# Optimization experiments

Measured on AMD Instinct MI355X. Metric: run time of the kernel, lower is better.

Reference implementation:

```python
import jax, jax.numpy as jnp
import numpy as np

N_NODES = 100000
N_EDGES = 1600000
IN_DIM, HID_DIM, OUT_DIM = 128, 32, 32


def setup_inputs() -> dict:
    key = jax.random.key(0)
    k1, k2, k3, k4, k5 = jax.random.split(key, 5)
    x = jax.random.normal(k1, (N_NODES, IN_DIM), dtype=jnp.float32)
    W1 = jax.random.normal(k2, (IN_DIM, HID_DIM), dtype=jnp.float32) * (1.0 / np.sqrt(IN_DIM))
    W2 = jax.random.normal(k3, (HID_DIM, OUT_DIM), dtype=jnp.float32) * (1.0 / np.sqrt(HID_DIM))
    edge_weight = jax.random.uniform(k4, (N_EDGES,), dtype=jnp.float32)
    edge_index = jax.random.randint(k5, (2, N_EDGES), 0, N_NODES, dtype=jnp.int64)
    return {"x": x, "W1": W1, "W2": W2, "edge_weight": edge_weight, "edge_index": edge_index}


def _gcn_conv(x, W, edge_index, edge_weight):
    # GCNConv with add_self_loops=False, normalize=False, bias=False:
    # h = x @ W ; out[dst] += edge_weight * h[src]
    src, dst = edge_index[0], edge_index[1]
    h = x @ W                                   # [N, out]
    msg = h[src] * edge_weight[:, None]         # [E, out] gather + scale
    return jax.ops.segment_sum(msg, dst, num_segments=x.shape[0])  # scatter-add


def reference(x, W1, W2, edge_weight, edge_index):
    h = _gcn_conv(x, W1, edge_index, edge_weight)   # no activation in source
    z = _gcn_conv(h, W2, edge_index, edge_weight)
    return z
```

## Files before the change

kernel.cpp:

```cpp
#include <hip/hip_runtime.h>

#define N_NODES 100000
#define N_EDGES 1600000
#define IN_DIM 128
#define HID_DIM 32

#define NPB 256
#define BSHIFT 8
#define NBUCK ((N_NODES + NPB - 1) / NPB)
#define EPB 4096
#define NBLK_E ((N_EDGES + EPB - 1) / EPB)
#define OSTRIDE (NBUCK + 1)
#define CAPB 4608
#define MMROWS 128
#define NBLK_MM ((N_NODES + MMROWS - 1) / MMROWS)
#define MM1 352
#define MM2 (NBLK_MM - MM1)
#define XS_STRIDE 136

typedef __attribute__((ext_vector_type(8))) short bf16x8;
typedef __attribute__((ext_vector_type(4))) float f32x4;

__device__ __forceinline__ unsigned int pack_bf16x2(float a0, float a1) {
    unsigned int u0 = __float_as_uint(a0), u1 = __float_as_uint(a1);
    u0 = (u0 + 0x7FFFu + ((u0 >> 16) & 1u)) >> 16;
    u1 = (u1 + 0x7FFFu + ((u1 >> 16) & 1u)) >> 16;
    return u0 | (u1 << 16);
}

__device__ __forceinline__ unsigned short bf16_of(float v) {
    unsigned int u = __float_as_uint(v);
    u = (u + 0x7FFFu + ((u >> 16) & 1u)) >> 16;
    return (unsigned short)u;
}

__device__ __forceinline__ int scan512(int v, int* wtmp) {
    const int t = threadIdx.x, lane = t & 63, wv = t >> 6;
    int incl = v;
#pragma unroll
    for (int o = 1; o < 64; o <<= 1) {
        const int n = __shfl_up(incl, o, 64);
        if (lane >= o) incl += n;
    }
    if (lane == 63) wtmp[wv] = incl;
    __syncthreads();
    if (t < 8) {
        const int wval = wtmp[t];
        int s = wval;
#pragma unroll
        for (int o = 1; o < 8; o <<= 1) {
            const int n = __shfl_up(s, o, 64);
            if (t >= o) s += n;
        }
        wtmp[t] = s - wval;
    }
    __syncthreads();
    return incl + wtmp[wv];
}

__device__ __forceinline__ void mm_body(char* smem, int row0,
                                        const float* __restrict__ x,
                                        const float* __restrict__ W,
                                        unsigned int* __restrict__ h) {
    const int tid = threadIdx.x;
    unsigned short* xbf = (unsigned short*)smem;
    const int lane = tid & 63, w = tid >> 6;

#pragma unroll
    for (int i = 0; i < 8; ++i) {
        const int idx = tid + i * 512;
        const int r = idx >> 5, c4 = idx & 31;
        const int grow = row0 + r;
        float4 vv = (grow < N_NODES) ? ((const float4*)x)[(size_t)grow * 32 + c4]
                                     : make_float4(0.f, 0.f, 0.f, 0.f);
        *(uint2*)&xbf[r * XS_STRIDE + c4 * 4] =
            make_uint2(pack_bf16x2(vv.x, vv.y), pack_bf16x2(vv.z, vv.w));
    }

    const int colB = lane & 15, kg = lane >> 4;
    bf16x8 bfrag[2][4];
#pragma unroll
    for (int n = 0; n < 2; ++n)
#pragma unroll
        for (int kt = 0; kt < 4; ++kt) {
            const int kbase = kt * 32 + kg * 8;
            bf16x8 f;
#pragma unroll
            for (int j = 0; j < 8; ++j)
                f[j] = (short)bf16_of(W[(size_t)(kbase + j) * HID_DIM + n * 16 + colB]);
            bfrag[n][kt] = f;
        }
    __syncthreads();

    f32x4 acc0 = {0.f, 0.f, 0.f, 0.f}, acc1 = {0.f, 0.f, 0.f, 0.f};
    const int arow = w * 16 + (lane & 15);
#pragma unroll
    for (int kt = 0; kt < 4; ++kt) {
        bf16x8 a = *(bf16x8*)&xbf[arow * XS_STRIDE + kt * 32 + kg * 8];
        acc0 = __builtin_amdgcn_mfma_f32_16x16x32_bf16(a, bfrag[0][kt], acc0, 0, 0, 0);
        acc1 = __builtin_amdgcn_mfma_f32_16x16x32_bf16(a, bfrag[1][kt], acc1, 0, 0, 0);
    }
    __syncthreads();

    float* cst = (float*)smem;
    float* cw_ = cst + w * 576;
    const int crow = (lane >> 4) * 4;
#pragma unroll
    for (int r = 0; r < 4; ++r) {
        cw_[(crow + r) * 36 + (lane & 15)] = acc0[r];
        cw_[(crow + r) * 36 + 16 + (lane & 15)] = acc1[r];
    }
    __syncthreads();
    const int r = tid >> 2, q = tid & 3;
    const int grow = row0 + r;
    if (grow < N_NODES) {
        const float* cr = cst + (r >> 4) * 576 + (r & 15) * 36 + q * 8;
        uint4 o = make_uint4(pack_bf16x2(cr[0], cr[1]), pack_bf16x2(cr[2], cr[3]),
                             pack_bf16x2(cr[4], cr[5]), pack_bf16x2(cr[6], cr[7]));
        ((uint4*)h)[(size_t)grow * 4 + q] = o;
    }
}

__global__ __launch_bounds__(512) void fusedA(const int* __restrict__ ei,
                                              const float* __restrict__ ew,
                                              unsigned int* __restrict__ ulin,
                                              unsigned short* __restrict__ wlin,
                                              int* __restrict__ ostart,
                                              const float* __restrict__ x,
                                              const float* __restrict__ W,
                                              unsigned int* __restrict__ h) {
    __shared__ __align__(16) char smem[36000];
    const int tid = threadIdx.x;

    if (blockIdx.x < NBLK_E) {
        unsigned int*   stag_u = (unsigned int*)smem;
        unsigned short* stag_w = (unsigned short*)(smem + 16384);
        int* lh     = (int*)(smem + 24576);
        int* lstart = (int*)(smem + 26144);
        int* wtmp   = (int*)(smem + 27712);

        for (int j = tid; j < NBUCK; j += 512) lh[j] = 0;
        __syncthreads();

        const int e0 = blockIdx.x * EPB;
        int dstr[8];
        unsigned int srcr[8];
        unsigned short wreg[8];
#pragma unroll
        for (int u = 0; u < 8; ++u) {
            const int e = e0 + u * 512 + tid;
            if (e < N_EDGES) {
                dstr[u] = ei[N_EDGES + e];
                srcr[u] = (unsigned int)ei[e];
                wreg[u] = bf16_of(ew[e]);
                atomicAdd(&lh[dstr[u] >> BSHIFT], 1);
            } else {
                dstr[u] = -1; srcr[u] = 0; wreg[u] = 0;
            }
        }
        __syncthreads();

        const int v = (tid < NBUCK) ? lh[tid] : 0;
        const int incl = scan512(v, wtmp);
        if (tid < NBUCK) lstart[tid] = incl - v;
        if (tid == NBUCK - 1) lstart[NBUCK] = incl;
        __syncthreads();
        if (tid < NBUCK) lh[tid] = 0;
        __syncthreads();

#pragma unroll
        for (int u = 0; u < 8; ++u) {
            const int d = dstr[u];
            if (d >= 0) {
                const int b = d >> BSHIFT;
                const int slot = atomicAdd(&lh[b], 1);
                const int p = lstart[b] + slot;
                stag_u[p] = srcr[u] | ((unsigned int)(d & (NPB - 1)) << 17);
                stag_w[p] = wreg[u];
            }
        }
        __syncthreads();

        const int total = lstart[NBUCK];
        const size_t gbase = (size_t)blockIdx.x * EPB;
        for (int i = tid; i < total; i += 512) {
            ulin[gbase + i] = stag_u[i];
            wlin[gbase + i] = stag_w[i];
        }
        if (tid < OSTRIDE) ostart[blockIdx.x * OSTRIDE + tid] = lstart[tid];
    } else {
        mm_body(smem, (int)(blockIdx.x - NBLK_E) * MMROWS, x, W, h);
    }
}

__global__ __launch_bounds__(512) void fusedB(const int* __restrict__ ostart,
                                              const unsigned int* __restrict__ ulin,
                                              const unsigned short* __restrict__ wlin,
                                              unsigned int* __restrict__ csr,
                                              int* __restrict__ offs,
                                              const float* __restrict__ x,
                                              const float* __restrict__ W,
                                              unsigned int* __restrict__ h) {
    __shared__ __align__(16) char smem[50304];
    const int t = threadIdx.x;

    if (blockIdx.x < NBUCK) {
        unsigned int*   stag_u = (unsigned int*)smem;
        unsigned short* stag_w = (unsigned short*)(smem + 18432);
        unsigned int*   stag2  = (unsigned int*)(smem + 27648);
        int* st   = (int*)(smem + 46080);
        int* P    = (int*)(smem + 47648);
        int* lh   = (int*)(smem + 49216);
        int* wtmp = (int*)(smem + 50240);
        const int b = blockIdx.x;

        int s0 = 0, len = 0;
        if (t < NBLK_E) {
            s0 = ostart[t * OSTRIDE + b];
            st[t] = s0;
            len = ostart[t * OSTRIDE + b + 1] - s0;
        }
        int* red = (int*)stag2;
        red[t] = s0;
        __syncthreads();
        for (int s = 256; s > 0; s >>= 1) {
            if (t < s) red[t] += red[t + s];
            __syncthreads();
        }
        const int base_out = red[0];
        __syncthreads();

        const int incl = scan512(len, wtmp);
        if (t < NBLK_E) P[t] = incl - len;
        if (t == NBLK_E - 1) P[NBLK_E] = incl;
        __syncthreads();
        const int cnt = min(P[NBLK_E], CAPB);

        for (int i = t; i < cnt; i += 512) {
            int lo = 0, hi = NBLK_E - 1;
            while (lo < hi) {
                const int mid = (lo + hi + 1) >> 1;
                if (P[mid] <= i) lo = mid; else hi = mid - 1;
            }
            const size_t g = (size_t)lo * EPB + st[lo] + (i - P[lo]);
            stag_u[i] = ulin[g];
            stag_w[i] = wlin[g];
        }
        if (t < NPB) lh[t] = 0;
        __syncthreads();

        for (int i = t; i < cnt; i += 512)
            atomicAdd(&lh[(stag_u[i] >> 17) & (NPB - 1)], 1);
        __syncthreads();

        const int v = (t < NPB) ? lh[t] : 0;
        const int incl2 = scan512(v, wtmp);
        if (t < NPB) {
            const int excl = incl2 - v;
            lh[t] = excl;
            const int node = (b << BSHIFT) + t;
            if (node < N_NODES) offs[node] = base_out + excl;
        }
        if (b == NBUCK - 1 && t == 0) offs[N_NODES] = base_out + cnt;
        __syncthreads();

        for (int i = t; i < cnt; i += 512) {
            const unsigned int u = stag_u[i];
            const int dl = (u >> 17) & (NPB - 1);
            const int pos = atomicAdd(&lh[dl], 1);
            stag2[pos] = (u & 0x1FFFF) | ((unsigned int)(stag_w[i] & 0x7FFFu) << 17);
        }
        __syncthreads();
        for (int i = t; i < cnt; i += 512) csr[base_out + i] = stag2[i];
    } else {
        mm_body(smem, (int)(blockIdx.x - NBUCK + MM1) * MMROWS, x, W, h);
    }
}


__device__ __forceinline__ void bf16fma8(float acc[8], const uint4 v, const float w) {
    acc[0] += w * __uint_as_float(v.x << 16);
    acc[1] += w * __uint_as_float(v.x & 0xFFFF0000u);
    acc[2] += w * __uint_as_float(v.y << 16);
    acc[3] += w * __uint_as_float(v.y & 0xFFFF0000u);
    acc[4] += w * __uint_as_float(v.z << 16);
    acc[5] += w * __uint_as_float(v.z & 0xFFFF0000u);
    acc[6] += w * __uint_as_float(v.w << 16);
    acc[7] += w * __uint_as_float(v.w & 0xFFFF0000u);
}

__device__ __forceinline__ void edge_accum(const int* __restrict__ offs,
                                           const unsigned int* __restrict__ csr,
                                           const uint4* __restrict__ h,
                                           int node, int ln, float acc[8]) {
    int i = offs[node];
    const int end = offs[node + 1];
    for (; i + 7 < end; i += 8) {
        unsigned int e[8];
        uint4 v[8];
#pragma unroll
        for (int j = 0; j < 8; ++j) e[j] = csr[i + j];
#pragma unroll
        for (int j = 0; j < 8; ++j) v[j] = h[(size_t)(e[j] & 0x1FFFF) * 4 + ln];
#pragma unroll
        for (int j = 0; j < 8; ++j)
            bf16fma8(acc, v[j], __uint_as_float((e[j] >> 17) << 16));
    }
    if (i + 3 < end) {
        unsigned int e[4];
        uint4 v[4];
#pragma unroll
        for (int j = 0; j < 4; ++j) e[j] = csr[i + j];
#pragma unroll
        for (int j = 0; j < 4; ++j) v[j] = h[(size_t)(e[j] & 0x1FFFF) * 4 + ln];
#pragma unroll
        for (int j = 0; j < 4; ++j)
            bf16fma8(acc, v[j], __uint_as_float((e[j] >> 17) << 16));
        i += 4;
    }
    for (; i < end; ++i) {
        const unsigned int e = csr[i];
        bf16fma8(acc, h[(size_t)(e & 0x1FFFF) * 4 + ln], __uint_as_float((e >> 17) << 16));
    }
}

__global__ __launch_bounds__(256) void gather_mm(const int* __restrict__ offs,
                                                 const unsigned int* __restrict__ csr,
                                                 const uint4* __restrict__ h1,
                                                 const float* __restrict__ W2,
                                                 uint4* __restrict__ h2) {
    __shared__ float W2s[HID_DIM * HID_DIM];
    __shared__ float a1s[64 * 33];
    const int tid = threadIdx.x;
    ((float4*)W2s)[tid] = ((const float4*)W2)[tid];
    const int g = tid >> 2, ln = tid & 3;
    const int node = blockIdx.x * 64 + g;
    const int node_c = min(node, N_NODES - 1);

    float acc[8] = {0.f, 0.f, 0.f, 0.f, 0.f, 0.f, 0.f, 0.f};
    edge_accum(offs, csr, h1, node_c, ln, acc);

    __syncthreads();
#pragma unroll
    for (int j = 0; j < 8; ++j) a1s[g * 33 + 8 * ln + j] = acc[j];
    __syncthreads();

    const float* ar = a1s + g * 33;
    float s[8] = {0.f, 0.f, 0.f, 0.f, 0.f, 0.f, 0.f, 0.f};
#pragma unroll
    for (int k = 0; k < HID_DIM; ++k) {
        const float av = ar[k];
        const float* wr = W2s + k * HID_DIM + 8 * ln;
#pragma unroll
        for (int j = 0; j < 8; ++j) s[j] += av * wr[j];
    }
    if (node < N_NODES)
        h2[(size_t)node * 4 + ln] = make_uint4(pack_bf16x2(s[0], s[1]),
                                               pack_bf16x2(s[2], s[3]),
                                               pack_bf16x2(s[4], s[5]),
                                               pack_bf16x2(s[6], s[7]));
}

__global__ __launch_bounds__(256) void gather_out(const int* __restrict__ offs,
                                                  const unsigned int* __restrict__ csr,
                                                  const uint4* __restrict__ h2,
                                                  float* __restrict__ out) {
    const int tid = threadIdx.x;
    const int g = tid >> 2, ln = tid & 3;
    const int node = blockIdx.x * 64 + g;
    if (node >= N_NODES) return;

    float acc[8] = {0.f, 0.f, 0.f, 0.f, 0.f, 0.f, 0.f, 0.f};
    edge_accum(offs, csr, h2, node, ln, acc);
    ((float4*)out)[(size_t)node * 8 + 2 * ln] = make_float4(acc[0], acc[1], acc[2], acc[3]);
    ((float4*)out)[(size_t)node * 8 + 2 * ln + 1] = make_float4(acc[4], acc[5], acc[6], acc[7]);
}

extern "C" void kernel_launch(void* const* d_in, const int* in_sizes, int n_in,
                              void* d_out, int out_size, void* d_ws, size_t ws_size,
                              hipStream_t stream) {
    const float* x  = (const float*)d_in[0];
    const float* W1 = (const float*)d_in[1];
    const float* W2 = (const float*)d_in[2];
    const float* ew = (const float*)d_in[3];
    const int*   ei = (const int*)d_in[4];
    float* out = (float*)d_out;

    unsigned int*   ulin = (unsigned int*)d_ws;
    unsigned short* wlin = (unsigned short*)(ulin + N_EDGES);
    unsigned int*   csr  = (unsigned int*)(wlin + N_EDGES);
    unsigned int*   h1u  = csr + N_EDGES;
    unsigned int*   h2u  = h1u + (size_t)N_NODES * 16;
    int*  offs   = (int*)(h2u + (size_t)N_NODES * 16);
    int*  ostart = offs + N_NODES + 1;

    fusedA<<<NBLK_E + MM1, 512, 0, stream>>>(ei, ew, ulin, wlin, ostart, x, W1, h1u);

    fusedB<<<NBUCK + MM2, 512, 0, stream>>>(ostart, ulin, wlin, csr, offs, x, W1, h1u);

    gather_mm<<<(N_NODES + 63) / 64, 256, 0, stream>>>(offs, csr, (const uint4*)h1u,
                                                       W2, (uint4*)h2u);

    gather_out<<<(N_NODES + 63) / 64, 256, 0, stream>>>(offs, csr, (const uint4*)h2u, out);
}
```

Baseline: 83.70 us.

## Split bf16 feature tables into two half-width arrays for gather passes

Stores the bf16 hidden features h1 and h2 as two separate 16-column halves (lo/hi, 32 bytes per node each) instead of one 64-byte row, and runs the edge gather twice, once per half. The goal is to shrink each half table's footprint so the random row gathers hit cache more often. In exchange the CSR edge list is read twice and each gather loads only 8 bytes per lane instead of 16.

```diff
diff --git a/kernel.cpp b/kernel.cpp
--- a/kernel.cpp
+++ b/kernel.cpp
@@ -61,7 +61,8 @@
 __device__ __forceinline__ void mm_body(char* smem, int row0,
                                         const float* __restrict__ x,
                                         const float* __restrict__ W,
-                                        unsigned int* __restrict__ h) {
+                                        unsigned int* __restrict__ hlo,
+                                        unsigned int* __restrict__ hhi) {
     const int tid = threadIdx.x;
     unsigned short* xbf = (unsigned short*)smem;
     const int lane = tid & 63, w = tid >> 6;
@@ -117,7 +118,8 @@
         const float* cr = cst + (r >> 4) * 576 + (r & 15) * 36 + q * 8;
         uint4 o = make_uint4(pack_bf16x2(cr[0], cr[1]), pack_bf16x2(cr[2], cr[3]),
                              pack_bf16x2(cr[4], cr[5]), pack_bf16x2(cr[6], cr[7]));
-        ((uint4*)h)[(size_t)grow * 4 + q] = o;
+        if (q < 2) ((uint4*)hlo)[(size_t)grow * 2 + q] = o;
+        else       ((uint4*)hhi)[(size_t)grow * 2 + q - 2] = o;
     }
 }
 
@@ -128,7 +130,8 @@
                                               int* __restrict__ ostart,
                                               const float* __restrict__ x,
                                               const float* __restrict__ W,
-                                              unsigned int* __restrict__ h) {
+                                              unsigned int* __restrict__ hlo,
+                                              unsigned int* __restrict__ hhi) {
     __shared__ __align__(16) char smem[36000];
     const int tid = threadIdx.x;
 
@@ -189,7 +192,7 @@
         }
         if (tid < OSTRIDE) ostart[blockIdx.x * OSTRIDE + tid] = lstart[tid];
     } else {
-        mm_body(smem, (int)(blockIdx.x - NBLK_E) * MMROWS, x, W, h);
+        mm_body(smem, (int)(blockIdx.x - NBLK_E) * MMROWS, x, W, hlo, hhi);
     }
 }
 
@@ -200,7 +203,8 @@
                                               int* __restrict__ offs,
                                               const float* __restrict__ x,
                                               const float* __restrict__ W,
-                                              unsigned int* __restrict__ h) {
+                                              unsigned int* __restrict__ hlo,
+                                              unsigned int* __restrict__ hhi) {
     __shared__ __align__(16) char smem[50304];
     const int t = threadIdx.x;
 
@@ -273,62 +277,57 @@
         __syncthreads();
         for (int i = t; i < cnt; i += 512) csr[base_out + i] = stag2[i];
     } else {
-        mm_body(smem, (int)(blockIdx.x - NBUCK + MM1) * MMROWS, x, W, h);
-    }
-}
-
-
-__device__ __forceinline__ void bf16fma8(float acc[8], const uint4 v, const float w) {
+        mm_body(smem, (int)(blockIdx.x - NBUCK + MM1) * MMROWS, x, W, hlo, hhi);
+    }
+}
+
+
+__device__ __forceinline__ void bf16fma4(float acc[4], const uint2 v, const float w) {
     acc[0] += w * __uint_as_float(v.x << 16);
     acc[1] += w * __uint_as_float(v.x & 0xFFFF0000u);
     acc[2] += w * __uint_as_float(v.y << 16);
     acc[3] += w * __uint_as_float(v.y & 0xFFFF0000u);
-    acc[4] += w * __uint_as_float(v.z << 16);
-    acc[5] += w * __uint_as_float(v.z & 0xFFFF0000u);
-    acc[6] += w * __uint_as_float(v.w << 16);
-    acc[7] += w * __uint_as_float(v.w & 0xFFFF0000u);
-}
-
-__device__ __forceinline__ void edge_accum(const int* __restrict__ offs,
-                                           const unsigned int* __restrict__ csr,
-                                           const uint4* __restrict__ h,
-                                           int node, int ln, float acc[8]) {
-    int i = offs[node];
-    const int end = offs[node + 1];
+}
+
+__device__ __forceinline__ void half_accum(const unsigned int* __restrict__ csr,
+                                           const uint2* __restrict__ hh,
+                                           int i, int end, int ln, float acc[4]) {
     for (; i + 7 < end; i += 8) {
         unsigned int e[8];
-        uint4 v[8];
+        uint2 v[8];
 #pragma unroll
         for (int j = 0; j < 8; ++j) e[j] = csr[i + j];
 #pragma unroll
-        for (int j = 0; j < 8; ++j) v[j] = h[(size_t)(e[j] & 0x1FFFF) * 4 + ln];
+        for (int j = 0; j < 8; ++j) v[j] = hh[(size_t)(e[j] & 0x1FFFF) * 4 + ln];
 #pragma unroll
         for (int j = 0; j < 8; ++j)
-            bf16fma8(acc, v[j], __uint_as_float((e[j] >> 17) << 16));
+            bf16fma4(acc, v[j], __uint_as_float((e[j] >> 17) << 16));
     }
     if (i + 3 < end) {
         unsigned int e[4];
-        uint4 v[4];
+        uint2 v[4];
 #pragma unroll
         for (int j = 0; j < 4; ++j) e[j] = csr[i + j];
 #pragma unroll
-        for (int j = 0; j < 4; ++j) v[j] = h[(size_t)(e[j] & 0x1FFFF) * 4 + ln];
+        for (int j = 0; j < 4; ++j) v[j] = hh[(size_t)(e[j] & 0x1FFFF) * 4 + ln];
 #pragma unroll
         for (int j = 0; j < 4; ++j)
-            bf16fma8(acc, v[j], __uint_as_float((e[j] >> 17) << 16));
+            bf16fma4(acc, v[j], __uint_as_float((e[j] >> 17) << 16));
         i += 4;
     }
     for (; i < end; ++i) {
         const unsigned int e = csr[i];
-        bf16fma8(acc, h[(size_t)(e & 0x1FFFF) * 4 + ln], __uint_as_float((e >> 17) << 16));
+        bf16fma4(acc, hh[(size_t)(e & 0x1FFFF) * 4 + ln], __uint_as_float((e >> 17) << 16));
     }
 }
 
 __global__ __launch_bounds__(256) void gather_mm(const int* __restrict__ offs,
                                                  const unsigned int* __restrict__ csr,
-                                                 const uint4* __restrict__ h1,
+                                                 const uint2* __restrict__ h1lo,
+                                                 const uint2* __restrict__ h1hi,
                                                  const float* __restrict__ W2,
-                                                 uint4* __restrict__ h2) {
+                                                 unsigned int* __restrict__ h2lo,
+                                                 unsigned int* __restrict__ h2hi) {
     __shared__ float W2s[HID_DIM * HID_DIM];
     __shared__ float a1s[64 * 33];
     const int tid = threadIdx.x;
@@ -336,13 +335,19 @@
     const int g = tid >> 2, ln = tid & 3;
     const int node = blockIdx.x * 64 + g;
     const int node_c = min(node, N_NODES - 1);
-
-    float acc[8] = {0.f, 0.f, 0.f, 0.f, 0.f, 0.f, 0.f, 0.f};
-    edge_accum(offs, csr, h1, node_c, ln, acc);
-
-    __syncthreads();
-#pragma unroll
-    for (int j = 0; j < 8; ++j) a1s[g * 33 + 8 * ln + j] = acc[j];
+    const int i0 = offs[node_c], end = offs[node_c + 1];
+
+    float aclo[4] = {0.f, 0.f, 0.f, 0.f};
+    float achi[4] = {0.f, 0.f, 0.f, 0.f};
+    half_accum(csr, h1lo, i0, end, ln, aclo);
+    half_accum(csr, h1hi, i0, end, ln, achi);
+
+    __syncthreads();
+#pragma unroll
+    for (int j = 0; j < 4; ++j) {
+        a1s[g * 33 + 4 * ln + j]      = aclo[j];
+        a1s[g * 33 + 16 + 4 * ln + j] = achi[j];
+    }
     __syncthreads();
 
     const float* ar = a1s + g * 33;
@@ -354,26 +359,32 @@
 #pragma unroll
         for (int j = 0; j < 8; ++j) s[j] += av * wr[j];
     }
-    if (node < N_NODES)
-        h2[(size_t)node * 4 + ln] = make_uint4(pack_bf16x2(s[0], s[1]),
-                                               pack_bf16x2(s[2], s[3]),
-                                               pack_bf16x2(s[4], s[5]),
-                                               pack_bf16x2(s[6], s[7]));
+    if (node < N_NODES) {
+        uint4 o = make_uint4(pack_bf16x2(s[0], s[1]), pack_bf16x2(s[2], s[3]),
+                             pack_bf16x2(s[4], s[5]), pack_bf16x2(s[6], s[7]));
+        if (ln < 2) ((uint4*)h2lo)[(size_t)node * 2 + ln] = o;
+        else        ((uint4*)h2hi)[(size_t)node * 2 + ln - 2] = o;
+    }
 }
 
 __global__ __launch_bounds__(256) void gather_out(const int* __restrict__ offs,
                                                   const unsigned int* __restrict__ csr,
-                                                  const uint4* __restrict__ h2,
+                                                  const uint2* __restrict__ h2lo,
+                                                  const uint2* __restrict__ h2hi,
                                                   float* __restrict__ out) {
     const int tid = threadIdx.x;
     const int g = tid >> 2, ln = tid & 3;
     const int node = blockIdx.x * 64 + g;
     if (node >= N_NODES) return;
-
-    float acc[8] = {0.f, 0.f, 0.f, 0.f, 0.f, 0.f, 0.f, 0.f};
-    edge_accum(offs, csr, h2, node, ln, acc);
-    ((float4*)out)[(size_t)node * 8 + 2 * ln] = make_float4(acc[0], acc[1], acc[2], acc[3]);
-    ((float4*)out)[(size_t)node * 8 + 2 * ln + 1] = make_float4(acc[4], acc[5], acc[6], acc[7]);
+    const int i0 = offs[node], end = offs[node + 1];
+
+    float aclo[4] = {0.f, 0.f, 0.f, 0.f};
+    float achi[4] = {0.f, 0.f, 0.f, 0.f};
+    half_accum(csr, h2lo, i0, end, ln, aclo);
+    half_accum(csr, h2hi, i0, end, ln, achi);
+
+    ((float4*)out)[(size_t)node * 8 + ln]     = make_float4(aclo[0], aclo[1], aclo[2], aclo[3]);
+    ((float4*)out)[(size_t)node * 8 + 4 + ln] = make_float4(achi[0], achi[1], achi[2], achi[3]);
 }
 
 extern "C" void kernel_launch(void* const* d_in, const int* in_sizes, int n_in,
@@ -389,17 +400,25 @@
     unsigned int*   ulin = (unsigned int*)d_ws;
     unsigned short* wlin = (unsigned short*)(ulin + N_EDGES);
     unsigned int*   csr  = (unsigned int*)(wlin + N_EDGES);
-    unsigned int*   h1u  = csr + N_EDGES;
-    unsigned int*   h2u  = h1u + (size_t)N_NODES * 16;
-    int*  offs   = (int*)(h2u + (size_t)N_NODES * 16);
+    unsigned int*   h1lo = csr + N_EDGES;
+    unsigned int*   h1hi = h1lo + (size_t)N_NODES * 8;
+    unsigned int*   h2lo = h1hi + (size_t)N_NODES * 8;
+    unsigned int*   h2hi = h2lo + (size_t)N_NODES * 8;
+    int*  offs   = (int*)(h2hi + (size_t)N_NODES * 8);
     int*  ostart = offs + N_NODES + 1;
 
-    fusedA<<<NBLK_E + MM1, 512, 0, stream>>>(ei, ew, ulin, wlin, ostart, x, W1, h1u);
-
-    fusedB<<<NBUCK + MM2, 512, 0, stream>>>(ostart, ulin, wlin, csr, offs, x, W1, h1u);
-
-    gather_mm<<<(N_NODES + 63) / 64, 256, 0, stream>>>(offs, csr, (const uint4*)h1u,
-                                                       W2, (uint4*)h2u);
-
-    gather_out<<<(N_NODES + 63) / 64, 256, 0, stream>>>(offs, csr, (const uint4*)h2u, out);
-}
+    fusedA<<<NBLK_E + MM1, 512, 0, stream>>>(ei, ew, ulin, wlin, ostart, x, W1,
+                                             h1lo, h1hi);
+
+    fusedB<<<NBUCK + MM2, 512, 0, stream>>>(ostart, ulin, wlin, csr, offs, x, W1,
+                                            h1lo, h1hi);
+
+    gather_mm<<<(N_NODES + 63) / 64, 256, 0, stream>>>(offs, csr,
+                                                       (const uint2*)h1lo,
+                                                       (const uint2*)h1hi,
+                                                       W2, h2lo, h2hi);
+
+    gather_out<<<(N_NODES + 63) / 64, 256, 0, stream>>>(offs, csr,
+                                                        (const uint2*)h2lo,
+                                                        (const uint2*)h2hi, out);
+}
```

Result: slower. 103.5 us (+23.6%).
